# Kernel tuning notes

Measured on AMD Instinct MI355X. Metric: run time of the kernel, lower is better.

Reference implementation:

```python
import jax, jax.numpy as jnp
import numpy as np

B, T, I, H, O = 4096, 512, 1, 64, 1


def setup_inputs() -> dict:
    key = jax.random.key(0)
    ks = jax.random.split(key, 7)
    s = 1.0 / np.sqrt(H)  # PyTorch default init scale
    return {
        "x": jax.random.normal(ks[0], (B, T, I), dtype=jnp.float32),
        "w_ih": jax.random.uniform(ks[1], (4 * H, I), jnp.float32, -s, s),
        "w_hh": jax.random.uniform(ks[2], (4 * H, H), jnp.float32, -s, s),
        "b_ih": jax.random.uniform(ks[3], (4 * H,), jnp.float32, -s, s),
        "b_hh": jax.random.uniform(ks[4], (4 * H,), jnp.float32, -s, s),
        "w_out": jax.random.uniform(ks[5], (O, H), jnp.float32, -s, s),
        "b_out": jax.random.uniform(ks[6], (O,), jnp.float32, -s, s),
    }


def reference(x, w_ih, w_hh, b_ih, b_hh, w_out, b_out):
    # x: [B, T, I]; PyTorch gate order in 4H dim is (i, f, g, o)
    b = b_ih + b_hh  # [4H]
    # precompute input projections for all timesteps: [T, B, 4H]
    xg = jnp.einsum("bti,gi->tbg", x, w_ih) + b

    def step(carry, xg_t):
        h, c = carry  # [B, H] each
        gates = xg_t + h @ w_hh.T  # [B, 4H]
        i, f, g, o = jnp.split(gates, 4, axis=-1)
        i = jax.nn.sigmoid(i)
        f = jax.nn.sigmoid(f)
        g = jnp.tanh(g)
        o = jax.nn.sigmoid(o)
        c = f * c + i * g
        h = o * jnp.tanh(c)
        return (h, c), None

    nb = x.shape[0]
    h0 = jnp.zeros((nb, w_hh.shape[1]), x.dtype)
    (h_T, _), _ = jax.lax.scan(step, (h0, h0), xg)
    # linear on last hidden state only (lstm_out[:, -1, :])
    return h_T @ w_out.T + b_out
```

## Files before the change

kernel.cpp:

```cpp
#include <hip/hip_runtime.h>


#define TT   512
#define MB   8
#define HP   72
#define BUFE (16 * HP)
#define SXP  10

#define L2E  1.4426950408889634f
#define L2E2 2.8853900817779268f

typedef _Float16 f16x8 __attribute__((ext_vector_type(8)));
typedef float    f32x4 __attribute__((ext_vector_type(4)));

#define MFMA16(a, b, c) __builtin_amdgcn_mfma_f32_16x16x32_f16((a), (b), (c), 0, 0, 0)

__device__ __forceinline__ float rcp_(float x)  { return __builtin_amdgcn_rcpf(x); }
__device__ __forceinline__ float exp2_(float x) { return __builtin_amdgcn_exp2f(x); }

__device__ __forceinline__ f16x8 cvt8s(const float4& u0, const float4& u1, float s) {
    f16x8 r;
    r[0] = (_Float16)(u0.x * s); r[1] = (_Float16)(u0.y * s);
    r[2] = (_Float16)(u0.z * s); r[3] = (_Float16)(u0.w * s);
    r[4] = (_Float16)(u1.x * s); r[5] = (_Float16)(u1.y * s);
    r[6] = (_Float16)(u1.z * s); r[7] = (_Float16)(u1.w * s);
    return r;
}

__global__ __launch_bounds__(256, 2) void lstm_mfma(
    const float* __restrict__ x,
    const float* __restrict__ w_ih,
    const float* __restrict__ w_hh,
    const float* __restrict__ b_ih,
    const float* __restrict__ b_hh,
    const float* __restrict__ w_out,
    const float* __restrict__ b_out,
    float* __restrict__ out)
{
    __shared__ __align__(16) float    sh_x[TT * SXP];
    __shared__ __align__(16) _Float16 hbuf[2 * BUFE];

    const int tid = threadIdx.x;
    const int w   = tid >> 6;
    const int L   = tid & 63;
    const int l16 = L & 15;
    const int h0  = L >> 4;
    const int b0  = blockIdx.x * MB;
    const int j   = 16 * w + l16;

    {
        const int q = tid >> 5;
        const int l = tid & 31;
        const float* xr = x + (size_t)(b0 + q) * TT;
        #pragma unroll
        for (int i = 0; i < TT / 32; ++i)
            sh_x[(l + 32 * i) * SXP + q] = xr[l + 32 * i];
    }
    for (int i = tid; i < 2 * BUFE; i += 256) hbuf[i] = (_Float16)0.0f;

    const float sc[4] = {-L2E, -L2E, L2E2, -L2E};
    f16x8 Bf[4][2];
    float wihv[4], biasv[4];
    #pragma unroll
    for (int s = 0; s < 4; ++s) {
        const int n = 64 * s + j;
        #pragma unroll
        for (int kt = 0; kt < 2; ++kt) {
            const float* p = w_hh + n * 64 + kt * 32 + h0 * 8;
            float4 u0 = *(const float4*)p;
            float4 u1 = *(const float4*)(p + 4);
            Bf[s][kt] = cvt8s(u0, u1, sc[s]);
        }
        wihv[s]  = w_ih[n] * sc[s];
        biasv[s] = (b_ih[n] + b_hh[n]) * sc[s];
    }

    const int aoff = l16 * HP + h0 * 8;
    const int xoff = 2 * h0;
    const int wr   = 4 * h0 * HP + j;

    float cc0 = 0.0f, cc1 = 0.0f;

    auto cellup = [&](float ai, float af, float ag, float ao, float& cc) -> float {
        float Ei = exp2_(ai), Ef = exp2_(af), Eg = exp2_(ag);
        float Di = 1.0f + Ei, Df = 1.0f + Ef, Dg = 1.0f + Eg;
        float Pif = Di * Df;
        float u   = rcp_(Pif * Dg);
        float si  = u * (Df * Dg);
        float sf  = u * (Di * Dg);
        float tg  = fmaf(-2.0f, u * Pif, 1.0f);
        cc = fmaf(sf, cc, si * tg);
        float Ec = exp2_(fminf(cc * L2E2, 64.0f));
        float Eo = exp2_(ao);
        float Dc = 1.0f + Ec, Do = 1.0f + Eo;
        float u2 = rcp_(Do * Dc);
        return (u2 * Dc) * fmaf(-2.0f, u2 * Do, 1.0f);
    };

    f32x4 ci[4];
    {
        const float2 x0 = *(const float2*)(sh_x + 0 * SXP + xoff);
        #pragma unroll
        for (int s = 0; s < 4; ++s) {
            ci[s][0] = fmaf(x0.x, wihv[s], biasv[s]);
            ci[s][1] = 0.0f;
            ci[s][2] = fmaf(x0.y, wihv[s], biasv[s]);
            ci[s][3] = 0.0f;
        }
    }

    __syncthreads();

    if (((blockIdx.x >> 8) ^ blockIdx.x) & 1) {
        __builtin_amdgcn_s_sleep(10);
    }

    auto step = [&](const _Float16* rb, _Float16* wb, int t) {
        f16x8 a0 = *(const f16x8*)(rb + aoff);
        f16x8 a1 = *(const f16x8*)(rb + aoff + 32);

        f32x4 acc[4];
        #pragma unroll
        for (int s = 0; s < 4; ++s)
            acc[s] = MFMA16(a1, Bf[s][1], MFMA16(a0, Bf[s][0], ci[s]));

        if (t + 1 < TT) {
            const float2 xn = *(const float2*)(sh_x + (t + 1) * SXP + xoff);
            #pragma unroll
            for (int s = 0; s < 4; ++s) {
                ci[s][0] = fmaf(xn.x, wihv[s], biasv[s]);
                ci[s][2] = fmaf(xn.y, wihv[s], biasv[s]);
            }
        }

        {
            float hv = cellup(acc[0][0] + acc[0][1], acc[1][0] + acc[1][1],
                              acc[2][0] + acc[2][1], acc[3][0] + acc[3][1], cc0);
            _Float16 hh = (_Float16)hv;
            wb[wr]      = hh;
            wb[wr + HP] = (_Float16)(hv - (float)hh);
        }
        {
            float hv = cellup(acc[0][2] + acc[0][3], acc[1][2] + acc[1][3],
                              acc[2][2] + acc[2][3], acc[3][2] + acc[3][3], cc1);
            _Float16 hh = (_Float16)hv;
            wb[wr + 2 * HP] = hh;
            wb[wr + 3 * HP] = (_Float16)(hv - (float)hh);
        }
        __syncthreads();
    };

    for (int t = 0; t < TT; t += 2) {
        step(hbuf,        hbuf + BUFE, t);
        step(hbuf + BUFE, hbuf,        t + 1);
    }

    const float wo = w_out[L];
    #pragma unroll
    for (int p = 0; p < 2; ++p) {
        const int q = 2 * w + p;
        float hvf = (float)hbuf[(2 * q) * HP + L] + (float)hbuf[(2 * q + 1) * HP + L];
        float v = hvf * wo;
        #pragma unroll
        for (int off = 32; off; off >>= 1) v += __shfl_down(v, off);
        if (L == 0) out[b0 + q] = v + b_out[0];
    }
}

extern "C" void kernel_launch(void* const* d_in, const int* in_sizes, int n_in,
                              void* d_out, int out_size, void* d_ws, size_t ws_size,
                              hipStream_t stream) {
    const float* x     = (const float*)d_in[0];
    const float* w_ih  = (const float*)d_in[1];
    const float* w_hh  = (const float*)d_in[2];
    const float* b_ih  = (const float*)d_in[3];
    const float* b_hh  = (const float*)d_in[4];
    const float* w_out = (const float*)d_in[5];
    const float* b_out = (const float*)d_in[6];
    float* out = (float*)d_out;

    lstm_mfma<<<4096 / MB, 256, 0, stream>>>(x, w_ih, w_hh, b_ih, b_hh,
                                             w_out, b_out, out);
}
```

Baseline: 328.8 us.

## Merge two batch groups per block with per-group LDS flag barriers

Each block now holds 16 batch rows split into two independent 256-thread groups, launched as 256 blocks of 512 threads. The per-step __syncthreads is replaced by a per-group LDS atomic counter that the four waves of a group spin on, so the two groups run their recurrences without waiting on each other. The second group starts slightly later via s_sleep so the two groups' phases are staggered. This costs atomic traffic and spin-waiting in exchange for avoiding block-wide barriers, and the exp clamp is lowered from 64 to 30.

Result: slower. 341.2 us (+3.8%).

```diff
diff --git a/kernel.cpp b/kernel.cpp
--- a/kernel.cpp
+++ b/kernel.cpp
@@ -2,10 +2,9 @@
 
 
 #define TT   512
-#define MB   8
 #define HP   72
 #define BUFE (16 * HP)
-#define SXP  10
+#define SXP  18
 
 #define L2E  1.4426950408889634f
 #define L2E2 2.8853900817779268f
@@ -27,7 +26,7 @@
     return r;
 }
 
-__global__ __launch_bounds__(256, 2) void lstm_mfma(
+__global__ __launch_bounds__(512, 2) void lstm_fs(
     const float* __restrict__ x,
     const float* __restrict__ w_ih,
     const float* __restrict__ w_hh,
@@ -38,15 +37,17 @@
     float* __restrict__ out)
 {
     __shared__ __align__(16) float    sh_x[TT * SXP];
-    __shared__ __align__(16) _Float16 hbuf[2 * BUFE];
+    __shared__ __align__(16) _Float16 hbuf[2][2][BUFE];
+    __shared__ unsigned int           flag[2];
 
     const int tid = threadIdx.x;
-    const int w   = tid >> 6;
+    const int g   = tid >> 8;
+    const int w4  = (tid >> 6) & 3;
     const int L   = tid & 63;
     const int l16 = L & 15;
     const int h0  = L >> 4;
-    const int b0  = blockIdx.x * MB;
-    const int j   = 16 * w + l16;
+    const int b0  = blockIdx.x * 16;
+    const int j   = 16 * w4 + l16;
 
     {
         const int q = tid >> 5;
@@ -56,7 +57,8 @@
         for (int i = 0; i < TT / 32; ++i)
             sh_x[(l + 32 * i) * SXP + q] = xr[l + 32 * i];
     }
-    for (int i = tid; i < 2 * BUFE; i += 256) hbuf[i] = (_Float16)0.0f;
+    for (int i = tid; i < 2 * 2 * BUFE; i += 512) (&hbuf[0][0][0])[i] = (_Float16)0.0f;
+    if (tid < 2) flag[tid] = 0u;
 
     const float sc[4] = {-L2E, -L2E, L2E2, -L2E};
     f16x8 Bf[4][2];
@@ -75,8 +77,8 @@
         biasv[s] = (b_ih[n] + b_hh[n]) * sc[s];
     }
 
-    const int aoff = l16 * HP + h0 * 8;
-    const int xoff = 2 * h0;
+    const int aoff = l16 * HP + 8 * h0;
+    const int xoff = 8 * g + 2 * h0;
     const int wr   = 4 * h0 * HP + j;
 
     float cc0 = 0.0f, cc1 = 0.0f;
@@ -90,16 +92,20 @@
         float sf  = u * (Di * Dg);
         float tg  = fmaf(-2.0f, u * Pif, 1.0f);
         cc = fmaf(sf, cc, si * tg);
-        float Ec = exp2_(fminf(cc * L2E2, 64.0f));
+        float Ec = exp2_(fminf(cc * L2E2, 30.0f));
         float Eo = exp2_(ao);
         float Dc = 1.0f + Ec, Do = 1.0f + Eo;
         float u2 = rcp_(Do * Dc);
         return (u2 * Dc) * fmaf(-2.0f, u2 * Do, 1.0f);
     };
 
+    __syncthreads();
+
+    if (g) __builtin_amdgcn_s_sleep(9);
+
     f32x4 ci[4];
     {
-        const float2 x0 = *(const float2*)(sh_x + 0 * SXP + xoff);
+        const float2 x0 = *(const float2*)(sh_x + xoff);
         #pragma unroll
         for (int s = 0; s < 4; ++s) {
             ci[s][0] = fmaf(x0.x, wihv[s], biasv[s]);
@@ -109,13 +115,10 @@
         }
     }
 
-    __syncthreads();
+    for (int t = 0; t < TT; ++t) {
+        const _Float16* rb = hbuf[g][t & 1];
+        _Float16*       wb = hbuf[g][(t + 1) & 1];
 
-    if (((blockIdx.x >> 8) ^ blockIdx.x) & 1) {
-        __builtin_amdgcn_s_sleep(10);
-    }
-
-    auto step = [&](const _Float16* rb, _Float16* wb, int t) {
         f16x8 a0 = *(const f16x8*)(rb + aoff);
         f16x8 a1 = *(const f16x8*)(rb + aoff + 32);
 
@@ -124,8 +127,9 @@
         for (int s = 0; s < 4; ++s)
             acc[s] = MFMA16(a1, Bf[s][1], MFMA16(a0, Bf[s][0], ci[s]));
 
-        if (t + 1 < TT) {
-            const float2 xn = *(const float2*)(sh_x + (t + 1) * SXP + xoff);
+        {
+            const int tn = (t + 1 < TT) ? (t + 1) : t;
+            const float2 xn = *(const float2*)(sh_x + tn * SXP + xoff);
             #pragma unroll
             for (int s = 0; s < 4; ++s) {
                 ci[s][0] = fmaf(xn.x, wihv[s], biasv[s]);
@@ -147,23 +151,29 @@
             wb[wr + 2 * HP] = hh;
             wb[wr + 3 * HP] = (_Float16)(hv - (float)hh);
         }
-        __syncthreads();
-    };
 
-    for (int t = 0; t < TT; t += 2) {
-        step(hbuf,        hbuf + BUFE, t);
-        step(hbuf + BUFE, hbuf,        t + 1);
+        __threadfence_block();
+        if (L == 0) atomicAdd(&flag[g], 1u);
+        const unsigned int tgt = 4u * (unsigned)(t + 1);
+        while (__hip_atomic_load(&flag[g], __ATOMIC_ACQUIRE,
+                                 __HIP_MEMORY_SCOPE_WORKGROUP) < tgt)
+            __builtin_amdgcn_s_sleep(1);
     }
 
+    __syncthreads();
+
+    const int W = tid >> 6;
     const float wo = w_out[L];
     #pragma unroll
     for (int p = 0; p < 2; ++p) {
-        const int q = 2 * w + p;
-        float hvf = (float)hbuf[(2 * q) * HP + L] + (float)hbuf[(2 * q + 1) * HP + L];
+        const int m  = 2 * W + p;
+        const int gm = m >> 3, q = m & 7;
+        float hvf = (float)hbuf[gm][0][(2 * q) * HP + L]
+                  + (float)hbuf[gm][0][(2 * q + 1) * HP + L];
         float v = hvf * wo;
         #pragma unroll
         for (int off = 32; off; off >>= 1) v += __shfl_down(v, off);
-        if (L == 0) out[b0 + q] = v + b_out[0];
+        if (L == 0) out[b0 + m] = v + b_out[0];
     }
 }
 
@@ -179,6 +189,6 @@
     const float* b_out = (const float*)d_in[6];
     float* out = (float*)d_out;
 
-    lstm_mfma<<<4096 / MB, 256, 0, stream>>>(x, w_ih, w_hh, b_ih, b_hh,
-                                             w_out, b_out, out);
+    lstm_fs<<<256, 512, 0, stream>>>(x, w_ih, w_hh, b_ih, b_hh,
+                                     w_out, b_out, out);
 }
```
